# Optimization experiments

Hardware: AMD Instinct MI355X
Metric: run time of the kernel (lower is better)

The kernel has to match this reference:

```python
import jax, jax.numpy as jnp
import numpy as np
import math

NUM_HEADS = 16
SEGMENT_SIZE = 128
DILATION = 2


def hilbert_map(seq_len: int) -> np.ndarray:
    """Boustrophedon ('Hilbert') permutation, matching the torch reference."""
    if seq_len <= 64:
        return np.arange(seq_len, dtype=np.int64)
    g = int(math.ceil(math.sqrt(seq_len)))
    fm = np.zeros(seq_len, dtype=np.int64)
    idx = 0
    for row in range(g):
        cols = range(g) if row % 2 == 0 else range(g - 1, -1, -1)
        for col in cols:
            lp = row * g + col
            if lp < seq_len and idx < seq_len:
                fm[lp] = idx
                idx += 1
    return fm


def setup_inputs() -> dict:
    key = jax.random.key(0)
    k1, k2, k3 = jax.random.split(key, 3)
    B, S, D = 2, 8192, 1024
    x = jax.random.normal(k1, (B, S, D), dtype=jnp.float32)
    W_qkv = jax.random.normal(k2, (D, 3 * D), dtype=jnp.float32) * 0.02
    W_out = jax.random.normal(k3, (D, D), dtype=jnp.float32) * 0.02
    return {"x": x, "W_qkv": W_qkv, "W_out": W_out}


def reference(x, W_qkv, W_out):
    B, S, Dm = x.shape
    H, Dh = NUM_HEADS, Dm // NUM_HEADS
    seg, dil = SEGMENT_SIZE, DILATION
    scale = Dh ** -0.5

    qkv = (x @ W_qkv).reshape(B, S, 3, H, Dh)
    q = jnp.transpose(qkv[:, :, 0], (0, 2, 1, 3))  # [B,H,S,Dh]
    k = jnp.transpose(qkv[:, :, 1], (0, 2, 1, 3))
    v = jnp.transpose(qkv[:, :, 2], (0, 2, 1, 3))

    # Hilbert reorder (active since S > 64)
    m = jnp.asarray(hilbert_map(S))
    q, k, v = q[:, :, m], k[:, :, m], v[:, :, m]

    # Vectorized segment-local dilated attention (S % seg == 0 here)
    nseg = S // seg
    qs = q.reshape(B, H, nseg, seg, Dh)
    ks = k.reshape(B, H, nseg, seg, Dh)[:, :, :, ::dil]  # dilated keys
    vs = v.reshape(B, H, nseg, seg, Dh)[:, :, :, ::dil]
    scores = jnp.einsum('bhnqd,bhnkd->bhnqk', qs, ks) * scale
    attn = jax.nn.softmax(scores, axis=-1)
    out = jnp.einsum('bhnqk,bhnkd->bhnqd', attn, vs).reshape(B, H, S, Dh)

    # Reverse Hilbert ordering
    inv = jnp.argsort(m)
    out = out[:, :, inv]

    out = jnp.transpose(out, (0, 2, 1, 3)).reshape(B, S, Dm)
    return out @ W_out
```

## Files before the change

### kernel.cpp

```cpp
#include <hip/hip_runtime.h>
#include <stdint.h>

typedef unsigned short ushort_t;
typedef __bf16 bf16x8 __attribute__((ext_vector_type(8)));
typedef float  f32x4  __attribute__((ext_vector_type(4)));

#define DEV static __device__ __forceinline__

DEV ushort_t f2bf(float f){
  union { float f; unsigned u; } x; x.f = f;
  unsigned u = x.u;
  return (ushort_t)((u + 0x7fffu + ((u >> 16) & 1u)) >> 16);
}

DEV int hmap(int p){
  int r = p / 91;
  int c = p - r * 91;
  return (r & 1) ? (r * 91 + 90 - c) : p;
}

DEV void async16(const void* g, void* l){
  __builtin_amdgcn_global_load_lds(
      (const __attribute__((address_space(1))) unsigned*)g,
      (__attribute__((address_space(3))) unsigned*)l, 16, 0, 0);
}

template<int GATHER>
DEV int arow_map(int r){
  if (GATHER == 0) return r;
  if (GATHER == 1){ int b = r >> 13, p = r & 8191; return b * 8192 + hmap(p); }
  int b = r >> 12, rem = r & 4095, seg = rem >> 6, j = rem & 63;
  return b * 8192 + hmap(seg * 128 + 2 * j);
}

__global__ void cast_kernel(const float* __restrict__ in, ushort_t* __restrict__ out, int n4){
  int i = blockIdx.x * blockDim.x + threadIdx.x;
  if (i < n4){
    float4 v = ((const float4*)in)[i];
    ushort4 o;
    o.x = f2bf(v.x); o.y = f2bf(v.y); o.z = f2bf(v.z); o.w = f2bf(v.w);
    ((ushort4*)out)[i] = o;
  }
}

__global__ void transpose_cast(const float* __restrict__ W, ushort_t* __restrict__ WT,
                               int rows, int cols){
  __shared__ ushort_t t[64 * 66];
  int tid = threadIdx.x;
  int c0 = blockIdx.x * 64, r0 = blockIdx.y * 64;
  int cl = tid & 63, rb = tid >> 6;
  for (int i = 0; i < 16; ++i){
    int r = rb + i * 4;
    t[r * 66 + cl] = f2bf(W[(size_t)(r0 + r) * cols + c0 + cl]);
  }
  __syncthreads();
  int rr = tid & 63, cb = tid >> 6;
  for (int i = 0; i < 16; ++i){
    int cc = cb + i * 4;
    WT[(size_t)(c0 + cc) * rows + r0 + rr] = t[rr * 66 + cc];
  }
}


#define BARRIER() asm volatile("s_barrier" ::: "memory")
#define LGKM0()   asm volatile("s_waitcnt lgkmcnt(0)" ::: "memory")
#define VMCNT4()  asm volatile("s_waitcnt vmcnt(4)" ::: "memory")
#define VMCNT0()  asm volatile("s_waitcnt vmcnt(0)" ::: "memory")

#define STAGE_A(T1, HT)                                                        \
  if ((T1) < NT){                                                              \
    ushort_t* d_ = &smem[((((T1) & 1)) << 15) + ((HT) << 13) + tid * 8];       \
    async16(&A[asrc[HT][0] + (size_t)(T1) * 64], d_);                          \
    async16(&A[asrc[HT][1] + (size_t)(T1) * 64], d_ + 4096);                   \
  }

#define STAGE_B(T2, HT)                                                        \
  if ((T2) < NT){                                                              \
    ushort_t* d_ = &smem[((((T2) & 1)) << 15) + 16384 + ((HT) << 13) + tid * 8];\
    async16(&BT[bsrc[HT][0] + (size_t)(T2) * 64], d_);                         \
    async16(&BT[bsrc[HT][1] + (size_t)(T2) * 64], d_ + 4096);                  \
  }

#define PHASE(MI0, STAGE_STMT, PRE_BAR2)                                       \
  {                                                                            \
    bf16x8 af[2][2];                                                           \
    _Pragma("unroll") for (int m2 = 0; m2 < 2; ++m2)                           \
      _Pragma("unroll") for (int kk = 0; kk < 2; ++kk)                         \
        af[m2][kk] = *(const bf16x8*)&Ab[((MI0) + m2) * 1024 + axor[kk]];      \
    STAGE_STMT;                                                                \
    BARRIER();                                                                 \
    LGKM0();                                                                   \
    __builtin_amdgcn_s_setprio(1);                                             \
    _Pragma("unroll") for (int kk = 0; kk < 2; ++kk)                           \
      _Pragma("unroll") for (int ni = 0; ni < 4; ++ni)                         \
        _Pragma("unroll") for (int m2 = 0; m2 < 2; ++m2)                       \
          acc[(MI0) + m2][ni] = __builtin_amdgcn_mfma_f32_16x16x32_bf16(       \
              af[m2][kk], bv[ni][kk], acc[(MI0) + m2][ni], 0, 0, 0);           \
    __builtin_amdgcn_s_setprio(0);                                             \
    PRE_BAR2;                                                                  \
    BARRIER();                                                                 \
  }

template<int OUT_BF16, int GATHER>
__global__ __launch_bounds__(512, 2) void gemm_bt(const ushort_t* __restrict__ A,
                                                  const ushort_t* __restrict__ BT,
                                                  void* __restrict__ Cout,
                                                  int M, int N, int K){
  __shared__ __align__(16) ushort_t smem[65536];
  const int NT = K >> 6;
  int tid = threadIdx.x;
  int lane = tid & 63, w = tid >> 6;
  int md = lane & 15, qd = lane >> 4;
  int wm = w >> 2, wn = w & 3;

  int nwg = gridDim.x;
  int orig = blockIdx.x;
  int wg = (orig & 7) * (nwg >> 3) + (orig >> 3);
  int mtc = M >> 8;
  int mt = wg % mtc, nt = wg / mtc;
  int m0 = mt << 8, n0 = nt << 8;

  int rbase = tid >> 3;
  int g0 = ((tid & 7) ^ (rbase & 7)) * 8;
  size_t asrc[2][2], bsrc[2][2];
  #pragma unroll
  for (int ht = 0; ht < 2; ++ht)
    #pragma unroll
    for (int i = 0; i < 2; ++i){
      asrc[ht][i] = (size_t)arow_map<GATHER>(m0 + ht * 128 + i * 64 + rbase) * K + g0;
      bsrc[ht][i] = (size_t)(n0 + ht * 128 + i * 64 + rbase) * K + g0;
    }

  int abase0 = (wm * 128 + md) * 64;
  int bbase0 = 16384 + (wn * 64 + md) * 64;
  int axor[2] = { (qd ^ (md & 7)) * 8, ((4 + qd) ^ (md & 7)) * 8 };

  f32x4 acc[8][4];
  #pragma unroll
  for (int a = 0; a < 8; ++a)
    #pragma unroll
    for (int b = 0; b < 4; ++b)
      #pragma unroll
      for (int e = 0; e < 4; ++e) acc[a][b][e] = 0.f;

  STAGE_B(0, 0); STAGE_B(0, 1);
  STAGE_A(0, 0); STAGE_A(0, 1);
  STAGE_B(1, 0); STAGE_B(1, 1);
  VMCNT4();
  BARRIER();

  for (int t = 0; t < NT; ++t){
    const ushort_t* Ab = &smem[((t & 1) << 15) + abase0];
    const ushort_t* Bb = &smem[((t & 1) << 15) + bbase0];

    bf16x8 bv[4][2];
    #pragma unroll
    for (int ni = 0; ni < 4; ++ni)
      #pragma unroll
      for (int kk = 0; kk < 2; ++kk)
        bv[ni][kk] = *(const bf16x8*)&Bb[ni * 1024 + axor[kk]];

    PHASE(0, STAGE_A(t + 1, 0), ((void)0));
    PHASE(2, STAGE_A(t + 1, 1), ((void)0));
    PHASE(4, STAGE_B(t + 2, 0), ((void)0));
    PHASE(6, STAGE_B(t + 2, 1),
          if (t < NT - 2) VMCNT4(); else VMCNT0());
  }

  int crow0 = m0 + wm * 128 + qd * 4;
  int ccol0 = n0 + wn * 64 + md;
  #pragma unroll
  for (int mi = 0; mi < 8; ++mi){
    #pragma unroll
    for (int ni = 0; ni < 4; ++ni){
      f32x4 v = acc[mi][ni];
      #pragma unroll
      for (int r = 0; r < 4; ++r){
        size_t idx = (size_t)(crow0 + mi * 16 + r) * N + ccol0 + ni * 16;
        if (OUT_BF16) ((ushort_t*)Cout)[idx] = f2bf(v[r]);
        else          ((float*)   Cout)[idx] = v[r];
      }
    }
  }
}

__global__ __launch_bounds__(256) void attn_kernel(const ushort_t* __restrict__ Qb,
                                                   const ushort_t* __restrict__ KV,
                                                   ushort_t* __restrict__ aout){
  __shared__ ushort_t Qs[128 * 72];
  __shared__ ushort_t Ks[64 * 72];
  __shared__ ushort_t Vt[64 * 72];
  int tid  = threadIdx.x;
  int lane = tid & 63, w = tid >> 6;
  int qd = lane >> 4, md = lane & 15;
  int seg = blockIdx.x, h = blockIdx.y, b = blockIdx.z;
  int p0 = seg * 128;

  for (int it = 0; it < 4; ++it){
    int q = it * 256 + tid;
    int r = q >> 3, ch = q & 7;
    uint4 d = *(const uint4*)&Qb[(size_t)(b * 8192 + p0 + r) * 1024 + h * 64 + ch * 8];
    *(uint4*)&Qs[r * 72 + ch * 8] = d;
  }
  for (int it = 0; it < 2; ++it){
    int q = it * 256 + tid;
    int r = q >> 3, ch = q & 7;
    uint4 d = *(const uint4*)&KV[(size_t)(b * 4096 + seg * 64 + r) * 2048 + h * 64 + ch * 8];
    *(uint4*)&Ks[r * 72 + ch * 8] = d;
  }
  for (int it = 0; it < 2; ++it){
    int q = it * 256 + tid;
    int r = q >> 3, ch = q & 7;
    union { uint4 v; ushort_t u[8]; } d;
    d.v = *(const uint4*)&KV[(size_t)(b * 4096 + seg * 64 + r) * 2048 + 1024 + h * 64 + ch * 8];
    for (int e = 0; e < 8; ++e) Vt[(ch * 8 + e) * 72 + r] = d.u[e];
  }
  __syncthreads();

  f32x4 z = {0.f, 0.f, 0.f, 0.f};
  f32x4 sc[2][4];
  for (int mi = 0; mi < 2; ++mi) for (int ni = 0; ni < 4; ++ni) sc[mi][ni] = z;
  for (int kc = 0; kc < 2; ++kc){
    bf16x8 aq[2], bk[4];
    for (int mi = 0; mi < 2; ++mi)
      aq[mi] = *(const bf16x8*)&Qs[(w * 32 + mi * 16 + md) * 72 + kc * 32 + qd * 8];
    for (int ni = 0; ni < 4; ++ni)
      bk[ni] = *(const bf16x8*)&Ks[(ni * 16 + md) * 72 + kc * 32 + qd * 8];
    for (int mi = 0; mi < 2; ++mi)
      for (int ni = 0; ni < 4; ++ni)
        sc[mi][ni] = __builtin_amdgcn_mfma_f32_16x16x32_bf16(aq[mi], bk[ni], sc[mi][ni], 0, 0, 0);
  }

  const float scale = 0.125f;
  ushort_t* Ps = Qs;
  for (int mi = 0; mi < 2; ++mi){
    for (int i = 0; i < 4; ++i){
      float mx = sc[mi][0][i];
      for (int ni = 1; ni < 4; ++ni) mx = fmaxf(mx, sc[mi][ni][i]);
      for (int d = 1; d < 16; d <<= 1) mx = fmaxf(mx, __shfl_xor(mx, d));
      float e[4], sum = 0.f;
      for (int ni = 0; ni < 4; ++ni){ e[ni] = __expf((sc[mi][ni][i] - mx) * scale); sum += e[ni]; }
      for (int d = 1; d < 16; d <<= 1) sum += __shfl_xor(sum, d);
      float inv = 1.0f / sum;
      int r = w * 32 + mi * 16 + qd * 4 + i;
      for (int ni = 0; ni < 4; ++ni)
        Ps[r * 72 + ni * 16 + md] = f2bf(e[ni] * inv);
    }
  }

  f32x4 oc[2][4];
  for (int mi = 0; mi < 2; ++mi) for (int ni = 0; ni < 4; ++ni) oc[mi][ni] = z;
  for (int kc = 0; kc < 2; ++kc){
    bf16x8 ap[2], bv[4];
    for (int mi = 0; mi < 2; ++mi)
      ap[mi] = *(const bf16x8*)&Ps[(w * 32 + mi * 16 + md) * 72 + kc * 32 + qd * 8];
    for (int ni = 0; ni < 4; ++ni)
      bv[ni] = *(const bf16x8*)&Vt[(ni * 16 + md) * 72 + kc * 32 + qd * 8];
    for (int mi = 0; mi < 2; ++mi)
      for (int ni = 0; ni < 4; ++ni)
        oc[mi][ni] = __builtin_amdgcn_mfma_f32_16x16x32_bf16(ap[mi], bv[ni], oc[mi][ni], 0, 0, 0);
  }

  for (int mi = 0; mi < 2; ++mi){
    for (int i = 0; i < 4; ++i){
      int rl = w * 32 + mi * 16 + qd * 4 + i;
      for (int ni = 0; ni < 4; ++ni)
        Ps[rl * 72 + ni * 16 + md] = f2bf(oc[mi][ni][i]);
    }
  }
  __syncthreads();
  for (int it = 0; it < 4; ++it){
    int q = it * 256 + tid;
    int r = q >> 3, ch = q & 7;
    int s = hmap(p0 + r);
    *(uint4*)&aout[(size_t)(b * 8192 + s) * 1024 + h * 64 + ch * 8] =
        *(const uint4*)&Qs[r * 72 + ch * 8];
  }
}

extern "C" void kernel_launch(void* const* d_in, const int* in_sizes, int n_in,
                              void* d_out, int out_size, void* d_ws, size_t ws_size,
                              hipStream_t stream){
  const float* x    = (const float*)d_in[0];
  const float* Wqkv = (const float*)d_in[1];
  const float* Wout = (const float*)d_in[2];
  float* out = (float*)d_out;

  char* ws = (char*)d_ws;
  ushort_t* xb    = (ushort_t*)(ws);
  ushort_t* WqT   = (ushort_t*)(ws + 33554432);
  ushort_t* WoT   = (ushort_t*)(ws + 39845888);
  ushort_t* Qbuf  = (ushort_t*)(ws + 41943040);
  ushort_t* KVbuf = (ushort_t*)(ws + 75497472);
  ushort_t* aoutb = (ushort_t*)(ws + 109051904);

  cast_kernel<<<16384, 256, 0, stream>>>(x, xb, (16384 * 1024) / 4);
  transpose_cast<<<dim3(48, 16), 256, 0, stream>>>(Wqkv, WqT, 1024, 3072);
  transpose_cast<<<dim3(16, 16), 256, 0, stream>>>(Wout, WoT, 1024, 1024);
  gemm_bt<1, 1><<<dim3(256), dim3(512), 0, stream>>>(xb, WqT, Qbuf, 16384, 1024, 1024);
  gemm_bt<1, 2><<<dim3(256), dim3(512), 0, stream>>>(xb, WqT + (size_t)1024 * 1024, KVbuf, 8192, 2048, 1024);
  attn_kernel<<<dim3(64, 16, 2), 256, 0, stream>>>(Qbuf, KVbuf, aoutb);
  gemm_bt<0, 0><<<dim3(256), dim3(512), 0, stream>>>(aoutb, WoT, out, 16384, 1024, 1024);
}
```

Before: 273.2 us.

## Replace async global-to-LDS staging with register-prefetch double buffering in GEMM

Swaps the global_load_lds direct-to-LDS staging and the four-phase interleaved MFMA schedule for a simpler pipeline. Each thread prefetches the tile two steps ahead into registers, writes it to the other LDS buffer after compute, and then synchronises once per K step. It also changes the workgroup-to-tile mapping so each XCD gets a contiguous band of M tiles across all N tiles. The aim is simpler synchronisation and better L2 locality, at the cost of extra VGPRs for the staging registers and less fine-grained overlap of loads with MFMA.

```diff
diff --git a/kernel.cpp b/kernel.cpp
--- a/kernel.cpp
+++ b/kernel.cpp
@@ -17,12 +17,6 @@
   int r = p / 91;
   int c = p - r * 91;
   return (r & 1) ? (r * 91 + 90 - c) : p;
-}
-
-DEV void async16(const void* g, void* l){
-  __builtin_amdgcn_global_load_lds(
-      (const __attribute__((address_space(1))) unsigned*)g,
-      (__attribute__((address_space(3))) unsigned*)l, 16, 0, 0);
 }
 
 template<int GATHER>
@@ -62,43 +56,24 @@
 }
 
 
+#define LGKM0()   asm volatile("s_waitcnt lgkmcnt(0)" ::: "memory")
 #define BARRIER() asm volatile("s_barrier" ::: "memory")
-#define LGKM0()   asm volatile("s_waitcnt lgkmcnt(0)" ::: "memory")
-#define VMCNT4()  asm volatile("s_waitcnt vmcnt(4)" ::: "memory")
-#define VMCNT0()  asm volatile("s_waitcnt vmcnt(0)" ::: "memory")
-
-#define STAGE_A(T1, HT)                                                        \
-  if ((T1) < NT){                                                              \
-    ushort_t* d_ = &smem[((((T1) & 1)) << 15) + ((HT) << 13) + tid * 8];       \
-    async16(&A[asrc[HT][0] + (size_t)(T1) * 64], d_);                          \
-    async16(&A[asrc[HT][1] + (size_t)(T1) * 64], d_ + 4096);                   \
-  }
-
-#define STAGE_B(T2, HT)                                                        \
-  if ((T2) < NT){                                                              \
-    ushort_t* d_ = &smem[((((T2) & 1)) << 15) + 16384 + ((HT) << 13) + tid * 8];\
-    async16(&BT[bsrc[HT][0] + (size_t)(T2) * 64], d_);                         \
-    async16(&BT[bsrc[HT][1] + (size_t)(T2) * 64], d_ + 4096);                  \
-  }
-
-#define PHASE(MI0, STAGE_STMT, PRE_BAR2)                                       \
+
+#define LOAD(T)                                                                \
   {                                                                            \
-    bf16x8 af[2][2];                                                           \
-    _Pragma("unroll") for (int m2 = 0; m2 < 2; ++m2)                           \
-      _Pragma("unroll") for (int kk = 0; kk < 2; ++kk)                         \
-        af[m2][kk] = *(const bf16x8*)&Ab[((MI0) + m2) * 1024 + axor[kk]];      \
-    STAGE_STMT;                                                                \
-    BARRIER();                                                                 \
-    LGKM0();                                                                   \
-    __builtin_amdgcn_s_setprio(1);                                             \
-    _Pragma("unroll") for (int kk = 0; kk < 2; ++kk)                           \
-      _Pragma("unroll") for (int ni = 0; ni < 4; ++ni)                         \
-        _Pragma("unroll") for (int m2 = 0; m2 < 2; ++m2)                       \
-          acc[(MI0) + m2][ni] = __builtin_amdgcn_mfma_f32_16x16x32_bf16(       \
-              af[m2][kk], bv[ni][kk], acc[(MI0) + m2][ni], 0, 0, 0);           \
-    __builtin_amdgcn_s_setprio(0);                                             \
-    PRE_BAR2;                                                                  \
-    BARRIER();                                                                 \
+    _Pragma("unroll") for (int i = 0; i < 4; ++i){                             \
+      ra[i] = *(const uint4*)&A [asrcR[i] + (size_t)(T) * 64];                 \
+      rb[i] = *(const uint4*)&BT[bsrcR[i] + (size_t)(T) * 64];                 \
+    }                                                                          \
+  }
+
+#define WRITE(T)                                                               \
+  {                                                                            \
+    ushort_t* d_ = &smem[(((T) & 1) << 15) + rbase * 64 + wsl];                \
+    _Pragma("unroll") for (int i = 0; i < 4; ++i){                             \
+      *(uint4*)&d_[i * 4096]         = ra[i];                                  \
+      *(uint4*)&d_[16384 + i * 4096] = rb[i];                                  \
+    }                                                                          \
   }
 
 template<int OUT_BF16, int GATHER>
@@ -113,27 +88,26 @@
   int md = lane & 15, qd = lane >> 4;
   int wm = w >> 2, wn = w & 3;
 
-  int nwg = gridDim.x;
   int orig = blockIdx.x;
-  int wg = (orig & 7) * (nwg >> 3) + (orig >> 3);
-  int mtc = M >> 8;
-  int mt = wg % mtc, nt = wg / mtc;
+  int xcd = orig & 7, local = orig >> 3;
+  int ntc = N >> 8;
+  int ls  = (ntc == 8) ? 3 : 2;
+  int nt  = local & (ntc - 1);
+  int mt  = xcd * (32 >> ls) + (local >> ls);
   int m0 = mt << 8, n0 = nt << 8;
 
-  int rbase = tid >> 3;
-  int g0 = ((tid & 7) ^ (rbase & 7)) * 8;
-  size_t asrc[2][2], bsrc[2][2];
+  int rbase = tid >> 3, cch = tid & 7;
+  int wsl = (cch ^ (rbase & 7)) * 8;
+  size_t asrcR[4], bsrcR[4];
   #pragma unroll
-  for (int ht = 0; ht < 2; ++ht)
-    #pragma unroll
-    for (int i = 0; i < 2; ++i){
-      asrc[ht][i] = (size_t)arow_map<GATHER>(m0 + ht * 128 + i * 64 + rbase) * K + g0;
-      bsrc[ht][i] = (size_t)(n0 + ht * 128 + i * 64 + rbase) * K + g0;
-    }
-
-  int abase0 = (wm * 128 + md) * 64;
-  int bbase0 = 16384 + (wn * 64 + md) * 64;
+  for (int i = 0; i < 4; ++i){
+    asrcR[i] = (size_t)arow_map<GATHER>(m0 + i * 64 + rbase) * K + cch * 8;
+    bsrcR[i] = (size_t)(n0 + i * 64 + rbase) * K + cch * 8;
+  }
+
   int axor[2] = { (qd ^ (md & 7)) * 8, ((4 + qd) ^ (md & 7)) * 8 };
+  int abase = (wm * 128 + md) * 64;
+  int bbase = 16384 + (wn * 64 + md) * 64;
 
   f32x4 acc[8][4];
   #pragma unroll
@@ -143,28 +117,35 @@
       #pragma unroll
       for (int e = 0; e < 4; ++e) acc[a][b][e] = 0.f;
 
-  STAGE_B(0, 0); STAGE_B(0, 1);
-  STAGE_A(0, 0); STAGE_A(0, 1);
-  STAGE_B(1, 0); STAGE_B(1, 1);
-  VMCNT4();
-  BARRIER();
+  uint4 ra[4], rb[4];
+
+  LOAD(0);
+  WRITE(0);
+  LOAD(1);
+  LGKM0(); BARRIER();
 
   for (int t = 0; t < NT; ++t){
-    const ushort_t* Ab = &smem[((t & 1) << 15) + abase0];
-    const ushort_t* Bb = &smem[((t & 1) << 15) + bbase0];
-
-    bf16x8 bv[4][2];
+    const ushort_t* Ab = &smem[((t & 1) << 15) + abase];
+    const ushort_t* Bb = &smem[((t & 1) << 15) + bbase];
+
     #pragma unroll
-    for (int ni = 0; ni < 4; ++ni)
-      #pragma unroll
-      for (int kk = 0; kk < 2; ++kk)
-        bv[ni][kk] = *(const bf16x8*)&Bb[ni * 1024 + axor[kk]];
-
-    PHASE(0, STAGE_A(t + 1, 0), ((void)0));
-    PHASE(2, STAGE_A(t + 1, 1), ((void)0));
-    PHASE(4, STAGE_B(t + 2, 0), ((void)0));
-    PHASE(6, STAGE_B(t + 2, 1),
-          if (t < NT - 2) VMCNT4(); else VMCNT0());
+    for (int kk = 0; kk < 2; ++kk){
+      bf16x8 bg[4];
+      #pragma unroll
+      for (int ni = 0; ni < 4; ++ni)
+        bg[ni] = *(const bf16x8*)&Bb[ni * 1024 + axor[kk]];
+      #pragma unroll
+      for (int mi = 0; mi < 8; ++mi){
+        bf16x8 af = *(const bf16x8*)&Ab[mi * 1024 + axor[kk]];
+        #pragma unroll
+        for (int ni = 0; ni < 4; ++ni)
+          acc[mi][ni] = __builtin_amdgcn_mfma_f32_16x16x32_bf16(af, bg[ni], acc[mi][ni], 0, 0, 0);
+      }
+    }
+
+    if (t + 1 < NT) WRITE(t + 1);
+    if (t + 2 < NT) LOAD(t + 2);
+    LGKM0(); BARRIER();
   }
 
   int crow0 = m0 + wm * 128 + qd * 4;
```

New measurement: 383.9 us. 1.41x slower.
